# Kernel tuning notes

Hardware: AMD Instinct MI355X
Metric: run time of the kernel (lower is better)

The kernel has to match this reference:

```python
import jax, jax.numpy as jnp
import numpy as np

N_EDGES = 8_388_608      # total synapses (flat weight vector length)
NUM_TYPES = 200          # number of unique edge types (ragged groups)
STRENGTH = 1e-3          # regularizer strength (cast to float32 as in the TF module)


def setup_inputs() -> dict:
    key = jax.random.key(0)
    k1, k2, k3 = jax.random.split(key, 3)
    # Edges pre-sorted by edge type -> contiguous segments (equivalent to the
    # RaggedTensor.from_value_rowids grouping built in __init__).
    segment_ids = jnp.sort(
        jax.random.randint(k1, (N_EDGES,), 0, NUM_TYPES, dtype=jnp.int32))
    x = jax.random.normal(k2, (N_EDGES,), dtype=jnp.float32)
    init_raw = jax.random.normal(k3, (N_EDGES,), dtype=jnp.float32)
    # __init__ sorts the initial weights within each edge-type group; since
    # segment_ids is already sorted, lexsort with segment_ids as the primary
    # key sorts values within each contiguous segment.
    order = jnp.lexsort((init_raw, segment_ids))
    initial_sorted = init_raw[order]
    return {"x": x, "initial_sorted": initial_sorted, "segment_ids": segment_ids}


def reference(x, initial_sorted, segment_ids):
    x = x.astype(jnp.float32)
    # Segmented sort of the current weights: primary key = edge type,
    # secondary key = value. Equivalent to tf.sort(x_i) per ragged group.
    order = jnp.lexsort((x, segment_ids))
    x_sorted = x[order]                       # [n_edges], sorted within each group
    diff = jnp.abs(x_sorted - initial_sorted)  # per-edge |sorted(x) - sorted(y)|
    sums = jax.ops.segment_sum(diff, segment_ids, num_segments=NUM_TYPES)
    counts = jax.ops.segment_sum(jnp.ones_like(diff), segment_ids,
                                 num_segments=NUM_TYPES)
    emd = sums / jnp.maximum(counts, 1.0)      # per-group Wasserstein-1 (mean L1)
    return jnp.mean(emd) * jnp.float32(STRENGTH)
```

## Files before the change

### kernel.cpp

```cpp
#include <hip/hip_runtime.h>
#include <hip/hip_bf16.h>

#define NSEG 200
#define STRENGTH 1e-3f
#define NFB 8192
#define FSCALE (8192.0f / 12.0f)
#define BT 1024
#define SPLIT 5
#define WINCAP 9728
#define EPT 10
#define PSTRIDE (NFB + 8)
#define PCH 8192

__device__ __forceinline__ int fbin_of(float v) {
    float t = (v + 6.0f) * FSCALE;
    int b = (int)floorf(t);
    return b < 0 ? 0 : (b > NFB - 1 ? NFB - 1 : b);
}

__global__ void k_bounds(const int* __restrict__ seg, int* __restrict__ seg_starts,
                         float* __restrict__ segSums, unsigned* __restrict__ gcur, int N) {
    int stride = gridDim.x * blockDim.x;
    int tid = blockIdx.x * blockDim.x + threadIdx.x;
    if (tid == 0) { seg_starts[0] = 0; seg_starts[NSEG] = N; }
    for (int k = tid; k < NSEG; k += stride) segSums[k] = 0.f;
    for (int k = tid; k < NSEG * 8; k += stride) gcur[k] = 0u;
    const int4* s4 = (const int4*)seg;
    int N4 = N >> 2;
    for (int i = tid; i < N4; i += stride) {
        int4 s = s4[i];
        int prev = (i == 0) ? s.x : seg[i * 4 - 1];
        if (s.x != prev) seg_starts[s.x] = i * 4;
        if (s.y != s.x) seg_starts[s.y] = i * 4 + 1;
        if (s.z != s.y) seg_starts[s.z] = i * 4 + 2;
        if (s.w != s.z) seg_starts[s.w] = i * 4 + 3;
    }
}

__global__ void __launch_bounds__(BT)
k_hist(const float* __restrict__ x, const int* __restrict__ seg_starts,
       unsigned short* __restrict__ pfxg, int* __restrict__ Bg, int* __restrict__ Bpos) {
    __shared__ unsigned h32[NFB];
    __shared__ unsigned wsum[16];
    __shared__ int nsh;
    int s = blockIdx.x;
    int t = threadIdx.x;
    int st = seg_starts[s], en = seg_starts[s + 1];
    int n = en - st;
    const float* xs = x + st;
    for (int k = t; k < NFB; k += BT) h32[k] = 0;
    __syncthreads();
    if (n > 0) {
        int head = min(n, (int)((4 - (st & 3)) & 3));
        for (int k = t; k < head; k += BT) atomicAdd(&h32[fbin_of(xs[k])], 1u);
        int nv = (n - head) >> 2;
        const float4* xs4 = (const float4*)(xs + head);
        for (int j = t; j < nv; j += BT) {
            float4 v = xs4[j];
            atomicAdd(&h32[fbin_of(v.x)], 1u);
            atomicAdd(&h32[fbin_of(v.y)], 1u);
            atomicAdd(&h32[fbin_of(v.z)], 1u);
            atomicAdd(&h32[fbin_of(v.w)], 1u);
        }
        for (int k = head + nv * 4 + t; k < n; k += BT) atomicAdd(&h32[fbin_of(xs[k])], 1u);
    }
    __syncthreads();
    unsigned wbuf[8]; unsigned run = 0;
    #pragma unroll
    for (int i = 0; i < 8; ++i) { unsigned c = h32[t * 8 + i]; wbuf[i] = run; run += c; }
    unsigned incl = run;
    for (int off = 1; off < 64; off <<= 1) {
        unsigned nv2 = __shfl_up(incl, off, 64);
        if ((t & 63) >= off) incl += nv2;
    }
    if ((t & 63) == 63) wsum[t >> 6] = incl;
    __syncthreads();
    unsigned wb = 0; int myw = t >> 6;
    #pragma unroll
    for (int j = 0; j < 16; ++j) wb += (j < myw) ? wsum[j] : 0u;
    unsigned pbase = wb + incl - run;
    unsigned short* pp = pfxg + (size_t)s * PSTRIDE;
    unsigned pk0 = (pbase + wbuf[0]) | ((pbase + wbuf[1]) << 16);
    unsigned pk1 = (pbase + wbuf[2]) | ((pbase + wbuf[3]) << 16);
    unsigned pk2 = (pbase + wbuf[4]) | ((pbase + wbuf[5]) << 16);
    unsigned pk3 = (pbase + wbuf[6]) | ((pbase + wbuf[7]) << 16);
    ((uint4*)pp)[t] = make_uint4(pk0, pk1, pk2, pk3);
    if (t == BT - 1) { pp[NFB] = (unsigned short)(pbase + run); nsh = (int)(pbase + run); }
    #pragma unroll
    for (int i = 0; i < 8; ++i) h32[t * 8 + i] = pbase + wbuf[i];
    __syncthreads();
    if (t == 0) { Bg[s * 8 + 0] = 0; Bg[s * 8 + SPLIT] = NFB; Bpos[s * 8 + 0] = 0; Bpos[s * 8 + SPLIT] = nsh; }
    if (t >= 1 && t < SPLIT) {
        int target = (int)(((long)t * nsh) / SPLIT);
        int lo = 0, hi = NFB - 1;
        while (lo < hi) { int mid = (lo + hi) >> 1; if ((int)h32[mid + 1] > target) hi = mid; else lo = mid + 1; }
        Bg[s * 8 + t] = lo;
        Bpos[s * 8 + t] = (int)h32[lo];
    }
}

__global__ void __launch_bounds__(1024)
k_part(const float* __restrict__ x, const int* __restrict__ seg_starts,
       const int* __restrict__ Bg, const int* __restrict__ Bpos,
       unsigned* __restrict__ gcur, float* __restrict__ part, int N) {
    __shared__ int sst[NSEG + 1];
    __shared__ unsigned hh[16][12];
    __shared__ int gb[10];
    __shared__ int sB[8];
    int t = threadIdx.x;
    for (int k = t; k < NSEG + 1; k += 1024) sst[k] = seg_starts[k];
    if (t < 192) ((unsigned*)hh)[t] = 0u;
    __syncthreads();
    int base = blockIdx.x * PCH;
    if (base >= N) return;
    int lo = 0, hi = NSEG - 1;
    while (lo < hi) { int mid = (lo + hi) >> 1; if (base < sst[mid + 1]) hi = mid; else lo = mid + 1; }
    int s0 = lo, bnd = sst[s0 + 1];
    if (t < 4) sB[t] = Bg[s0 * 8 + 1 + t];
    else if (t < 8) sB[t] = Bg[(s0 + 1) * 8 + 1 + (t - 4)];
    __syncthreads();
    int grp = t >> 6;
    float vv[8]; unsigned pk[8];
    const float4* x4 = (const float4*)(x + base);
    #pragma unroll
    for (int it = 0; it < 2; ++it) {
        int j = it * 1024 + t;
        int gi = base + j * 4;
        float4 v4;
        if (gi + 3 < N) v4 = x4[j];
        else v4 = make_float4(0.f, 0.f, 0.f, 0.f);
        #pragma unroll
        for (int e = 0; e < 4; ++e) {
            int i = it * 4 + e;
            float v = (e == 0) ? v4.x : (e == 1) ? v4.y : (e == 2) ? v4.z : v4.w;
            vv[i] = v;
            int g = gi + e;
            if (g < N) {
                int off = (g >= bnd) ? 4 : 0;
                int f = fbin_of(v);
                int p = (f >= sB[off]) + (f >= sB[off + 1]) + (f >= sB[off + 2]) + (f >= sB[off + 3]);
                int sp = (off >> 2) * 5 + p;
                unsigned lr = atomicAdd(&hh[grp][sp], 1u);
                pk[i] = ((unsigned)sp << 10) | lr;
            } else pk[i] = 0xffffffffu;
        }
    }
    __syncthreads();
    if (t < 10) {
        unsigned run = 0;
        #pragma unroll
        for (int g = 0; g < 16; ++g) { unsigned c = hh[g][t]; hh[g][t] = run; run += c; }
        int s = s0 + (t >= 5);
        int p = (t >= 5) ? t - 5 : t;
        int rsv = 0;
        if (run > 0) rsv = (int)atomicAdd(&gcur[s * 8 + p], run);
        gb[t] = sst[s] + Bpos[s * 8 + p] + rsv;
    }
    __syncthreads();
    #pragma unroll
    for (int i = 0; i < 8; ++i) {
        if (pk[i] == 0xffffffffu) continue;
        int sp = (int)(pk[i] >> 10);
        int lr = (int)(pk[i] & 1023u);
        part[gb[sp] + (int)hh[grp][sp] + lr] = vv[i];
    }
}

__global__ void __launch_bounds__(BT)
k_seg(const float* __restrict__ part, const float* __restrict__ y,
      const int* __restrict__ seg_starts, const unsigned short* __restrict__ pfxg,
      const int* __restrict__ Bg, float* __restrict__ segSums) {
    __shared__ __align__(16) unsigned short pfx[NFB + 2];
    __shared__ unsigned cur[NFB / 4];
    __shared__ __align__(16) float win[WINCAP + 4];
    __shared__ float warr[16];
    int s = blockIdx.x % NSEG;
    int p = blockIdx.x / NSEG;
    int t = threadIdx.x;
    int st = seg_starts[s], en = seg_starts[s + 1];
    int n = en - st;
    if (n <= 0) return;
    const unsigned short* pp = pfxg + (size_t)s * PSTRIDE;
    ((uint4*)pfx)[t] = ((const uint4*)pp)[t];
    if (t == 0) pfx[NFB] = pp[NFB];
    __syncthreads();
    int Fa = Bg[s * 8 + p], Fb = Bg[s * 8 + p + 1];
    int w0 = (int)pfx[Fa], w1 = (int)pfx[Fb];
    int wsz = w1 - w0;
    int wA = Fa >> 2;
    int wB2 = (Fb > Fa) ? (((Fb - 1) >> 2) + 1) : wA;
    for (int k = wA + t; k < wB2; k += BT) cur[k] = 0u;
    __syncthreads();
    const float* ps = part + st + w0;
    int head = min(wsz, (int)((4 - ((st + w0) & 3)) & 3));
    for (int k = t; k < head; k += BT) {
        float v = ps[k];
        int f = fbin_of(v);
        unsigned shf = (f & 3) * 8;
        unsigned old = atomicAdd(&cur[f >> 2], 1u << shf);
        win[(int)pfx[f] - w0 + (int)((old >> shf) & 0xFFu)] = v;
    }
    int nv = (wsz - head) >> 2;
    const float4* ps4 = (const float4*)(ps + head);
    for (int j = t; j < nv; j += BT) {
        float4 v4 = ps4[j];
        #pragma unroll
        for (int e = 0; e < 4; ++e) {
            float v = (e == 0) ? v4.x : (e == 1) ? v4.y : (e == 2) ? v4.z : v4.w;
            int f = fbin_of(v);
            unsigned shf = (f & 3) * 8;
            unsigned old = atomicAdd(&cur[f >> 2], 1u << shf);
            win[(int)pfx[f] - w0 + (int)((old >> shf) & 0xFFu)] = v;
        }
    }
    for (int k = head + nv * 4 + t; k < wsz; k += BT) {
        float v = ps[k];
        int f = fbin_of(v);
        unsigned shf = (f & 3) * 8;
        unsigned old = atomicAdd(&cur[f >> 2], 1u << shf);
        win[(int)pfx[f] - w0 + (int)((old >> shf) & 0xFFu)] = v;
    }
    if (t < 4) win[wsz + t] = __builtin_inff();
    __syncthreads();
    float rv[EPT]; int rr[EPT];
    #pragma unroll
    for (int e = 0; e < EPT; ++e) {
        int ql = e * BT + t;
        rr[e] = -1;
        if (ql < wsz) {
            float v = win[ql];
            rv[e] = v;
            int f = fbin_of(v);
            int bs = (int)pfx[f], be = (int)pfx[f + 1];
            int ls = bs - w0, le = be - w0;
            int a = ls & ~3;
            int cnt = a - ls;
            for (int j = a; j < le; j += 4) {
                float4 qv = *(const float4*)&win[j];
                cnt += (qv.x < v) + ((qv.x == v) & (j + 0 < ql));
                cnt += (qv.y < v) + ((qv.y == v) & (j + 1 < ql));
                cnt += (qv.z < v) + ((qv.z == v) & (j + 2 < ql));
                cnt += (qv.w < v) + ((qv.w == v) & (j + 3 < ql));
            }
            rr[e] = ls + cnt;
        }
    }
    __syncthreads();
    #pragma unroll
    for (int e = 0; e < EPT; ++e) {
        if (rr[e] >= 0) win[rr[e]] = rv[e];
    }
    __syncthreads();
    float acc = 0.f;
    const float* yw = y + st + w0;
    int head2 = min(wsz, (int)((4 - ((st + w0) & 3)) & 3));
    for (int k = t; k < head2; k += BT) acc += fabsf(win[k] - yw[k]);
    int nv2 = (wsz - head2) >> 2;
    const float4* yw4 = (const float4*)(yw + head2);
    for (int j = t; j < nv2; j += BT) {
        float4 yv = yw4[j];
        int k = head2 + j * 4;
        acc += fabsf(win[k + 0] - yv.x);
        acc += fabsf(win[k + 1] - yv.y);
        acc += fabsf(win[k + 2] - yv.z);
        acc += fabsf(win[k + 3] - yv.w);
    }
    for (int k = head2 + nv2 * 4 + t; k < wsz; k += BT) acc += fabsf(win[k] - yw[k]);

    for (int off = 32; off > 0; off >>= 1) acc += __shfl_xor(acc, off, 64);
    if ((t & 63) == 0) warr[t >> 6] = acc;
    __syncthreads();
    if (t == 0) {
        float tot = 0.f;
        #pragma unroll
        for (int j = 0; j < 16; ++j) tot += warr[j];
        if (tot != 0.f) atomicAdd(&segSums[s], tot);
    }
}

__global__ void k_final(const float* __restrict__ segSums, const int* __restrict__ seg_starts,
                        float* __restrict__ out) {
    __shared__ float red[256];
    int t = threadIdx.x;
    float a = 0.f;
    for (int k = t; k < NSEG; k += 256) {
        float n = (float)(seg_starts[k + 1] - seg_starts[k]);
        a += segSums[k] / fmaxf(n, 1.0f);
    }
    red[t] = a;
    __syncthreads();
    for (int off = 128; off > 0; off >>= 1) {
        if (t < off) red[t] += red[t + off];
        __syncthreads();
    }
    if (t == 0) out[0] = red[0] * (1.0f / (float)NSEG) * STRENGTH;
}

extern "C" void kernel_launch(void* const* d_in, const int* in_sizes, int n_in,
                              void* d_out, int out_size, void* d_ws, size_t ws_size,
                              hipStream_t stream) {
    const float* x = (const float*)d_in[0];
    const float* y = (const float*)d_in[1];
    const int* seg = (const int*)d_in[2];
    int N = in_sizes[0];

    char* ws = (char*)d_ws;
    float* segSums    = (float*)ws;
    int*   seg_starts = (int*)(ws + 800);
    unsigned* gcur    = (unsigned*)(ws + 1616);
    int*   Bg         = (int*)(ws + 8016);
    int*   Bpos       = (int*)(ws + 14448);
    unsigned short* pfxg = (unsigned short*)(ws + 20880);
    float* part       = (float*)(ws + 20880 + (size_t)NSEG * PSTRIDE * 2 + 16);

    int nchunk = (N + PCH - 1) / PCH;

    k_bounds<<<512, 256, 0, stream>>>(seg, seg_starts, segSums, gcur, N);
    k_hist<<<NSEG, BT, 0, stream>>>(x, seg_starts, pfxg, Bg, Bpos);
    k_part<<<nchunk, 1024, 0, stream>>>(x, seg_starts, Bg, Bpos, gcur, part, N);
    k_seg<<<NSEG * SPLIT, BT, 0, stream>>>(part, y, seg_starts, pfxg, Bg, segSums);
    k_final<<<1, 256, 0, stream>>>(segSums, seg_starts, (float*)d_out);
}
```

Before: 103.0 us.

## Fuse segment-bound search into histogram, double fine bins, slice prefix in sort

Drops the separate k_bounds pass over the segment-id array. Each histogram block now finds its own segment start and end by binary search and clears the shared state itself. The fine histogram doubles to 16384 bins, stored as packed 16-bit counters so shared memory use stays the same, which should shrink the per-bin rank-counting work in k_seg. k_seg now loads only the slice of the prefix array covering its split range, and falls back to an all-pairs rank count when the slice is too large. The costs are serial binary searches on global memory at kernel start, and reliance on segment sizes fitting in 16-bit offsets.

```diff
diff --git a/kernel.cpp b/kernel.cpp
--- a/kernel.cpp
+++ b/kernel.cpp
@@ -3,14 +3,15 @@
 
 #define NSEG 200
 #define STRENGTH 1e-3f
-#define NFB 8192
-#define FSCALE (8192.0f / 12.0f)
+#define NFB 16384
+#define FSCALE (16384.0f / 12.0f)
 #define BT 1024
 #define SPLIT 5
 #define WINCAP 9728
 #define EPT 10
 #define PSTRIDE (NFB + 8)
 #define PCH 8192
+#define SLICE_E 8200
 
 __device__ __forceinline__ int fbin_of(float v) {
     float t = (v + 6.0f) * FSCALE;
@@ -18,56 +19,54 @@
     return b < 0 ? 0 : (b > NFB - 1 ? NFB - 1 : b);
 }
 
-__global__ void k_bounds(const int* __restrict__ seg, int* __restrict__ seg_starts,
-                         float* __restrict__ segSums, unsigned* __restrict__ gcur, int N) {
-    int stride = gridDim.x * blockDim.x;
-    int tid = blockIdx.x * blockDim.x + threadIdx.x;
-    if (tid == 0) { seg_starts[0] = 0; seg_starts[NSEG] = N; }
-    for (int k = tid; k < NSEG; k += stride) segSums[k] = 0.f;
-    for (int k = tid; k < NSEG * 8; k += stride) gcur[k] = 0u;
-    const int4* s4 = (const int4*)seg;
-    int N4 = N >> 2;
-    for (int i = tid; i < N4; i += stride) {
-        int4 s = s4[i];
-        int prev = (i == 0) ? s.x : seg[i * 4 - 1];
-        if (s.x != prev) seg_starts[s.x] = i * 4;
-        if (s.y != s.x) seg_starts[s.y] = i * 4 + 1;
-        if (s.z != s.y) seg_starts[s.z] = i * 4 + 2;
-        if (s.w != s.z) seg_starts[s.w] = i * 4 + 3;
-    }
-}
-
 __global__ void __launch_bounds__(BT)
-k_hist(const float* __restrict__ x, const int* __restrict__ seg_starts,
-       unsigned short* __restrict__ pfxg, int* __restrict__ Bg, int* __restrict__ Bpos) {
-    __shared__ unsigned h32[NFB];
+k_hist(const float* __restrict__ x, const int* __restrict__ seg,
+       int* __restrict__ seg_starts, float* __restrict__ segSums,
+       unsigned* __restrict__ gcur, unsigned short* __restrict__ pfxg,
+       int* __restrict__ Bg, int* __restrict__ Bpos, int N) {
+    __shared__ unsigned hw[NFB / 2];
     __shared__ unsigned wsum[16];
-    __shared__ int nsh;
+    __shared__ int sh2[3];
     int s = blockIdx.x;
     int t = threadIdx.x;
-    int st = seg_starts[s], en = seg_starts[s + 1];
+    if (t <= 1) {
+        int key = s + t;
+        int lo = 0, hi = N;
+        while (lo < hi) { int mid = (lo + hi) >> 1; if (seg[mid] < key) lo = mid + 1; else hi = mid; }
+        sh2[t] = lo;
+    }
+    if (t < 8) gcur[s * 8 + t] = 0u;
+    if (t == 2) segSums[s] = 0.f;
+    for (int k = t; k < NFB / 2; k += BT) hw[k] = 0;
+    __syncthreads();
+    int st = sh2[0], en = sh2[1];
+    if (t == 3) { seg_starts[s] = st; if (s == NSEG - 1) seg_starts[NSEG] = N; }
     int n = en - st;
     const float* xs = x + st;
-    for (int k = t; k < NFB; k += BT) h32[k] = 0;
-    __syncthreads();
     if (n > 0) {
         int head = min(n, (int)((4 - (st & 3)) & 3));
-        for (int k = t; k < head; k += BT) atomicAdd(&h32[fbin_of(xs[k])], 1u);
+        for (int k = t; k < head; k += BT) { int f = fbin_of(xs[k]); atomicAdd(&hw[f >> 1], 1u << ((f & 1) * 16)); }
         int nv = (n - head) >> 2;
         const float4* xs4 = (const float4*)(xs + head);
         for (int j = t; j < nv; j += BT) {
             float4 v = xs4[j];
-            atomicAdd(&h32[fbin_of(v.x)], 1u);
-            atomicAdd(&h32[fbin_of(v.y)], 1u);
-            atomicAdd(&h32[fbin_of(v.z)], 1u);
-            atomicAdd(&h32[fbin_of(v.w)], 1u);
-        }
-        for (int k = head + nv * 4 + t; k < n; k += BT) atomicAdd(&h32[fbin_of(xs[k])], 1u);
-    }
-    __syncthreads();
-    unsigned wbuf[8]; unsigned run = 0;
-    #pragma unroll
-    for (int i = 0; i < 8; ++i) { unsigned c = h32[t * 8 + i]; wbuf[i] = run; run += c; }
+            int f0 = fbin_of(v.x), f1 = fbin_of(v.y), f2 = fbin_of(v.z), f3 = fbin_of(v.w);
+            atomicAdd(&hw[f0 >> 1], 1u << ((f0 & 1) * 16));
+            atomicAdd(&hw[f1 >> 1], 1u << ((f1 & 1) * 16));
+            atomicAdd(&hw[f2 >> 1], 1u << ((f2 & 1) * 16));
+            atomicAdd(&hw[f3 >> 1], 1u << ((f3 & 1) * 16));
+        }
+        for (int k = head + nv * 4 + t; k < n; k += BT) { int f = fbin_of(xs[k]); atomicAdd(&hw[f >> 1], 1u << ((f & 1) * 16)); }
+    }
+    __syncthreads();
+    unsigned wv[8]; unsigned run = 0;
+    #pragma unroll
+    for (int i = 0; i < 8; ++i) {
+        unsigned w = hw[t * 8 + i];
+        unsigned c0 = w & 0xffffu, c1 = w >> 16;
+        wv[i] = run | ((run + c0) << 16);
+        run += c0 + c1;
+    }
     unsigned incl = run;
     for (int off = 1; off < 64; off <<= 1) {
         unsigned nv2 = __shfl_up(incl, off, 64);
@@ -78,24 +77,29 @@
     unsigned wb = 0; int myw = t >> 6;
     #pragma unroll
     for (int j = 0; j < 16; ++j) wb += (j < myw) ? wsum[j] : 0u;
-    unsigned pbase = wb + incl - run;
+    unsigned base = wb + incl - run;
+    unsigned bb = base | (base << 16);
     unsigned short* pp = pfxg + (size_t)s * PSTRIDE;
-    unsigned pk0 = (pbase + wbuf[0]) | ((pbase + wbuf[1]) << 16);
-    unsigned pk1 = (pbase + wbuf[2]) | ((pbase + wbuf[3]) << 16);
-    unsigned pk2 = (pbase + wbuf[4]) | ((pbase + wbuf[5]) << 16);
-    unsigned pk3 = (pbase + wbuf[6]) | ((pbase + wbuf[7]) << 16);
-    ((uint4*)pp)[t] = make_uint4(pk0, pk1, pk2, pk3);
-    if (t == BT - 1) { pp[NFB] = (unsigned short)(pbase + run); nsh = (int)(pbase + run); }
-    #pragma unroll
-    for (int i = 0; i < 8; ++i) h32[t * 8 + i] = pbase + wbuf[i];
-    __syncthreads();
+    #pragma unroll
+    for (int i = 0; i < 8; ++i) {
+        unsigned pw = wv[i] + bb;
+        hw[t * 8 + i] = pw;
+        ((unsigned*)pp)[t * 8 + i] = pw;
+    }
+    if (t == BT - 1) { pp[NFB] = (unsigned short)(base + run); sh2[2] = (int)(base + run); }
+    __syncthreads();
+    int nsh = sh2[2];
     if (t == 0) { Bg[s * 8 + 0] = 0; Bg[s * 8 + SPLIT] = NFB; Bpos[s * 8 + 0] = 0; Bpos[s * 8 + SPLIT] = nsh; }
     if (t >= 1 && t < SPLIT) {
         int target = (int)(((long)t * nsh) / SPLIT);
         int lo = 0, hi = NFB - 1;
-        while (lo < hi) { int mid = (lo + hi) >> 1; if ((int)h32[mid + 1] > target) hi = mid; else lo = mid + 1; }
+        while (lo < hi) {
+            int mid = (lo + hi) >> 1;
+            int pv = (int)((hw[(mid + 1) >> 1] >> (((mid + 1) & 1) * 16)) & 0xffffu);
+            if (pv > target) hi = mid; else lo = mid + 1;
+        }
         Bg[s * 8 + t] = lo;
-        Bpos[s * 8 + t] = (int)h32[lo];
+        Bpos[s * 8 + t] = (int)((hw[lo >> 1] >> ((lo & 1) * 16)) & 0xffffu);
     }
 }
 
@@ -117,7 +121,7 @@
     while (lo < hi) { int mid = (lo + hi) >> 1; if (base < sst[mid + 1]) hi = mid; else lo = mid + 1; }
     int s0 = lo, bnd = sst[s0 + 1];
     if (t < 4) sB[t] = Bg[s0 * 8 + 1 + t];
-    else if (t < 8) sB[t] = Bg[(s0 + 1) * 8 + 1 + (t - 4)];
+    else if (t < 8 && s0 + 1 <= NSEG) sB[t] = Bg[(s0 + 1) * 8 + 1 + (t - 4)];
     __syncthreads();
     int grp = t >> 6;
     float vv[8]; unsigned pk[8];
@@ -170,8 +174,8 @@
 k_seg(const float* __restrict__ part, const float* __restrict__ y,
       const int* __restrict__ seg_starts, const unsigned short* __restrict__ pfxg,
       const int* __restrict__ Bg, float* __restrict__ segSums) {
-    __shared__ __align__(16) unsigned short pfx[NFB + 2];
-    __shared__ unsigned cur[NFB / 4];
+    __shared__ unsigned short slice[SLICE_E];
+    __shared__ unsigned cur[2056];
     __shared__ __align__(16) float win[WINCAP + 4];
     __shared__ float warr[16];
     int s = blockIdx.x % NSEG;
@@ -181,68 +185,91 @@
     int n = en - st;
     if (n <= 0) return;
     const unsigned short* pp = pfxg + (size_t)s * PSTRIDE;
-    ((uint4*)pfx)[t] = ((const uint4*)pp)[t];
-    if (t == 0) pfx[NFB] = pp[NFB];
-    __syncthreads();
     int Fa = Bg[s * 8 + p], Fb = Bg[s * 8 + p + 1];
-    int w0 = (int)pfx[Fa], w1 = (int)pfx[Fb];
+    int spanc = Fb - Fa;
+    int w0 = pp[Fa], w1 = pp[Fb];
     int wsz = w1 - w0;
-    int wA = Fa >> 2;
-    int wB2 = (Fb > Fa) ? (((Fb - 1) >> 2) + 1) : wA;
-    for (int k = wA + t; k < wB2; k += BT) cur[k] = 0u;
-    __syncthreads();
+    if (wsz <= 0) return;
     const float* ps = part + st + w0;
-    int head = min(wsz, (int)((4 - ((st + w0) & 3)) & 3));
-    for (int k = t; k < head; k += BT) {
-        float v = ps[k];
-        int f = fbin_of(v);
-        unsigned shf = (f & 3) * 8;
-        unsigned old = atomicAdd(&cur[f >> 2], 1u << shf);
-        win[(int)pfx[f] - w0 + (int)((old >> shf) & 0xFFu)] = v;
-    }
-    int nv = (wsz - head) >> 2;
-    const float4* ps4 = (const float4*)(ps + head);
-    for (int j = t; j < nv; j += BT) {
-        float4 v4 = ps4[j];
-        #pragma unroll
-        for (int e = 0; e < 4; ++e) {
-            float v = (e == 0) ? v4.x : (e == 1) ? v4.y : (e == 2) ? v4.z : v4.w;
-            int f = fbin_of(v);
-            unsigned shf = (f & 3) * 8;
-            unsigned old = atomicAdd(&cur[f >> 2], 1u << shf);
-            win[(int)pfx[f] - w0 + (int)((old >> shf) & 0xFFu)] = v;
-        }
-    }
-    for (int k = head + nv * 4 + t; k < wsz; k += BT) {
-        float v = ps[k];
-        int f = fbin_of(v);
-        unsigned shf = (f & 3) * 8;
-        unsigned old = atomicAdd(&cur[f >> 2], 1u << shf);
-        win[(int)pfx[f] - w0 + (int)((old >> shf) & 0xFFu)] = v;
-    }
-    if (t < 4) win[wsz + t] = __builtin_inff();
-    __syncthreads();
+    bool sliced = (spanc + 1) <= SLICE_E;
+
     float rv[EPT]; int rr[EPT];
-    #pragma unroll
-    for (int e = 0; e < EPT; ++e) {
-        int ql = e * BT + t;
-        rr[e] = -1;
-        if (ql < wsz) {
-            float v = win[ql];
-            rv[e] = v;
-            int f = fbin_of(v);
-            int bs = (int)pfx[f], be = (int)pfx[f + 1];
-            int ls = bs - w0, le = be - w0;
-            int a = ls & ~3;
-            int cnt = a - ls;
-            for (int j = a; j < le; j += 4) {
-                float4 qv = *(const float4*)&win[j];
-                cnt += (qv.x < v) + ((qv.x == v) & (j + 0 < ql));
-                cnt += (qv.y < v) + ((qv.y == v) & (j + 1 < ql));
-                cnt += (qv.z < v) + ((qv.z == v) & (j + 2 < ql));
-                cnt += (qv.w < v) + ((qv.w == v) & (j + 3 < ql));
+    if (sliced) {
+        for (int k = t; k <= spanc; k += BT) slice[k] = pp[Fa + k];
+        for (int k = t; k < ((spanc + 4) >> 2); k += BT) cur[k] = 0u;
+        __syncthreads();
+        int head = min(wsz, (int)((4 - ((st + w0) & 3)) & 3));
+        for (int k = t; k < head; k += BT) {
+            float v = ps[k];
+            int i = fbin_of(v) - Fa;
+            unsigned shf = (i & 3) * 8;
+            unsigned old = atomicAdd(&cur[i >> 2], 1u << shf);
+            win[(int)slice[i] - w0 + (int)((old >> shf) & 0xFFu)] = v;
+        }
+        int nv = (wsz - head) >> 2;
+        const float4* ps4 = (const float4*)(ps + head);
+        for (int j = t; j < nv; j += BT) {
+            float4 v4 = ps4[j];
+            #pragma unroll
+            for (int e = 0; e < 4; ++e) {
+                float v = (e == 0) ? v4.x : (e == 1) ? v4.y : (e == 2) ? v4.z : v4.w;
+                int i = fbin_of(v) - Fa;
+                unsigned shf = (i & 3) * 8;
+                unsigned old = atomicAdd(&cur[i >> 2], 1u << shf);
+                win[(int)slice[i] - w0 + (int)((old >> shf) & 0xFFu)] = v;
             }
-            rr[e] = ls + cnt;
+        }
+        for (int k = head + nv * 4 + t; k < wsz; k += BT) {
+            float v = ps[k];
+            int i = fbin_of(v) - Fa;
+            unsigned shf = (i & 3) * 8;
+            unsigned old = atomicAdd(&cur[i >> 2], 1u << shf);
+            win[(int)slice[i] - w0 + (int)((old >> shf) & 0xFFu)] = v;
+        }
+        if (t < 4) win[wsz + t] = __builtin_inff();
+        __syncthreads();
+        #pragma unroll
+        for (int e = 0; e < EPT; ++e) {
+            int ql = e * BT + t;
+            rr[e] = -1;
+            if (ql < wsz) {
+                float v = win[ql];
+                rv[e] = v;
+                int i = fbin_of(v) - Fa;
+                int ls = (int)slice[i] - w0, le = (int)slice[i + 1] - w0;
+                int a = ls & ~3;
+                int cnt = a - ls;
+                for (int j = a; j < le; j += 4) {
+                    float4 qv = *(const float4*)&win[j];
+                    cnt += (qv.x < v) + ((qv.x == v) & (j + 0 < ql));
+                    cnt += (qv.y < v) + ((qv.y == v) & (j + 1 < ql));
+                    cnt += (qv.z < v) + ((qv.z == v) & (j + 2 < ql));
+                    cnt += (qv.w < v) + ((qv.w == v) & (j + 3 < ql));
+                }
+                rr[e] = ls + cnt;
+            }
+        }
+    } else {
+        for (int k = t; k < wsz; k += BT) win[k] = ps[k];
+        if (t < 4) win[wsz + t] = __builtin_inff();
+        __syncthreads();
+        #pragma unroll
+        for (int e = 0; e < EPT; ++e) {
+            int ql = e * BT + t;
+            rr[e] = -1;
+            if (ql < wsz) {
+                float v = win[ql];
+                rv[e] = v;
+                int cnt = 0;
+                for (int j = 0; j < wsz; j += 4) {
+                    float4 qv = *(const float4*)&win[j];
+                    cnt += (qv.x < v) + ((qv.x == v) & (j + 0 < ql));
+                    cnt += (qv.y < v) + ((qv.y == v) & (j + 1 < ql));
+                    cnt += (qv.z < v) + ((qv.z == v) & (j + 2 < ql));
+                    cnt += (qv.w < v) + ((qv.w == v) & (j + 3 < ql));
+                }
+                rr[e] = cnt;
+            }
         }
     }
     __syncthreads();
@@ -315,8 +342,7 @@
 
     int nchunk = (N + PCH - 1) / PCH;
 
-    k_bounds<<<512, 256, 0, stream>>>(seg, seg_starts, segSums, gcur, N);
-    k_hist<<<NSEG, BT, 0, stream>>>(x, seg_starts, pfxg, Bg, Bpos);
+    k_hist<<<NSEG, BT, 0, stream>>>(x, seg, seg_starts, segSums, gcur, pfxg, Bg, Bpos, N);
     k_part<<<nchunk, 1024, 0, stream>>>(x, seg_starts, Bg, Bpos, gcur, part, N);
     k_seg<<<NSEG * SPLIT, BT, 0, stream>>>(part, y, seg_starts, pfxg, Bg, segSums);
     k_final<<<1, 256, 0, stream>>>(segSums, seg_starts, (float*)d_out);
```

After: 89.89 us. -12.7%, faster.
